# Optimization experiments

Hardware: AMD Instinct MI355X
Metric: run time of the kernel (lower is better)

The kernel has to match this reference:

```python
import jax, jax.numpy as jnp
import numpy as np

HIDDEN = 1024
HEADS = 16
DK = HIDDEN // HEADS  # 64
B, N = 2, 2048


def setup_inputs() -> dict:
    key = jax.random.key(0)
    ks = jax.random.split(key, 12)
    s = 0.02
    return {
        "q": jax.random.normal(ks[0], (B, N, HIDDEN), jnp.float32),
        "k": jax.random.normal(ks[1], (B, N, HIDDEN), jnp.float32),
        "v": jax.random.normal(ks[2], (B, N, HIDDEN), jnp.float32),
        "attn_bias": jax.random.normal(ks[3], (B, N, N), jnp.float32),
        "attention_mask": jnp.zeros((B, N, N), jnp.float32),
        # projection weights stored [in, out]
        "Wq": jax.random.normal(ks[4], (HIDDEN, HIDDEN), jnp.float32) * s,
        "bq": jnp.zeros((HIDDEN,), jnp.float32),
        "Wk": jax.random.normal(ks[5], (HIDDEN, HIDDEN), jnp.float32) * s,
        "bk": jnp.zeros((HIDDEN,), jnp.float32),
        "Wv": jax.random.normal(ks[6], (HIDDEN, HIDDEN), jnp.float32) * s,
        "bv": jnp.zeros((HIDDEN,), jnp.float32),
        "Wo": jax.random.normal(ks[7], (HIDDEN, HIDDEN), jnp.float32) * s,
        "bo": jnp.zeros((HIDDEN,), jnp.float32),
    }


def reference(q, k, v, attn_bias, attention_mask, Wq, bq, Wk, bk, Wv, bv, Wo, bo):
    b, n, _ = q.shape
    scale = DK ** (-0.5)
    # project and split heads: [B, H, N, Dk]
    qh = (q @ Wq + bq).reshape(b, n, HEADS, DK).transpose(0, 2, 1, 3)
    kh = (k @ Wk + bk).reshape(b, -1, HEADS, DK).transpose(0, 2, 1, 3)
    vh = (v @ Wv + bv).reshape(b, -1, HEADS, DK).transpose(0, 2, 1, 3)
    # scaled scores + additive bias/mask broadcast over heads: [B, H, N, N]
    scores = jnp.einsum('bhnd,bhmd->bhnm', qh * scale, kh)
    scores = scores + attn_bias[:, None, :, :] + attention_mask[:, None, :, :]
    probs = jax.nn.softmax(scores, axis=-1)  # dropout is identity at inference
    ctx = jnp.einsum('bhnm,bhmd->bhnd', probs, vh)
    ctx = ctx.transpose(0, 2, 1, 3).reshape(b, n, HEADS * DK)
    return ctx @ Wo + bo
```

## Files before the change

kernel.cpp:

```cpp
#include <hip/hip_runtime.h>
#include <hip/hip_bf16.h>

#define HIDDEN 1024
#define NHEADS 16
#define DKH   64
#define BATCH 2
#define SEQ   2048
#define MTOT  (BATCH*SEQ)

using bf16x8 = __attribute__((ext_vector_type(8))) short;
using f32x4  = __attribute__((ext_vector_type(4))) float;
using u16x4  = __attribute__((ext_vector_type(4))) unsigned short;

__device__ __forceinline__ unsigned short f2bf(float f) {
    union { __hip_bfloat16 h; unsigned short u; } v;
    v.h = __float2bfloat16(f);
    return v.u;
}

__device__ __forceinline__ float asfloat(unsigned int u) {
    union { unsigned int u; float f; } v; v.u = u; return v.f;
}

__device__ __forceinline__ float fexp2(float x) {
#if __has_builtin(__builtin_amdgcn_exp2f)
    return __builtin_amdgcn_exp2f(x);
#else
    return exp2f(x);
#endif
}

__device__ __forceinline__ void gload16(const unsigned short* g, unsigned short* l) {
    __builtin_amdgcn_global_load_lds((const __attribute__((address_space(1))) void*)g,
                                     (__attribute__((address_space(3))) void*)l, 16, 0, 0);
}

#define L2E 1.44269504088896340736f

__global__ __launch_bounds__(256) void prep(const float* __restrict__ Wq,
                                            const float* __restrict__ Wk,
                                            const float* __restrict__ Wv,
                                            const float* __restrict__ Wo,
                                            unsigned short* __restrict__ wt,
                                            const float* __restrict__ bias,
                                            const float* __restrict__ mask,
                                            unsigned short* __restrict__ biasf) {
    __shared__ __align__(16) char sh[16640];
    float (*tile)[65] = (float (*)[65])sh;
    unsigned short (*lb)[520] = (unsigned short (*)[520])sh;
    const int bid = blockIdx.x, t = threadIdx.x;
    if (bid >= 1024) {
        int r = bid - 1024;
        const int z = r >> 8; r &= 255;
        const int kb = (r >> 4) * 64, nb = (r & 15) * 64;
        const float* W = (z == 0) ? Wq : (z == 1) ? Wk : (z == 2) ? Wv : Wo;
        unsigned short* out = wt + (size_t)z * HIDDEN * HIDDEN;
        #pragma unroll
        for (int i = 0; i < 16; i++) {
            int idx = i * 256 + t; int rr = idx >> 6, c = idx & 63;
            tile[rr][c] = W[(size_t)(kb + rr) * HIDDEN + nb + c];
        }
        __syncthreads();
        #pragma unroll
        for (int i = 0; i < 16; i++) {
            int idx = i * 256 + t; int n = idx >> 6, kk = idx & 63;
            out[(size_t)(nb + n) * HIDDEN + kb + kk] = f2bf(tile[kk][n]);
        }
    } else {
        const int cb = bid;
        const int chunk = cb & 3, g = (cb >> 2) & 127, b = cb >> 9;
        const float* bp = bias + ((size_t)b * SEQ + g * 16) * SEQ + chunk * 512;
        const float* mp = mask + ((size_t)b * SEQ + g * 16) * SEQ + chunk * 512;
        #pragma unroll
        for (int i = 0; i < 8; i++) {
            int idx = i * 256 + t;
            int row = idx >> 7, c4 = (idx & 127) * 4;
            float4 bv4 = *(const float4*)(bp + (size_t)row * SEQ + c4);
            float4 mv4 = *(const float4*)(mp + (size_t)row * SEQ + c4);
            union { u16x4 v; unsigned short s[4]; } o;
            o.s[0] = f2bf((bv4.x + mv4.x) * L2E);
            o.s[1] = f2bf((bv4.y + mv4.y) * L2E);
            o.s[2] = f2bf((bv4.z + mv4.z) * L2E);
            o.s[3] = f2bf((bv4.w + mv4.w) * L2E);
            *(u16x4*)&lb[row][c4] = o.v;
        }
        __syncthreads();
        const int w = t >> 6, ln = t & 63;
        const int quad = ln >> 4, c16 = ln & 15;
        unsigned short* ob = biasf + (((size_t)b * 128 + g) * 64 + chunk * 16) * 512 + ln * 8;
        #pragma unroll
        for (int it = 0; it < 4; it++) {
            int ttl = it * 4 + w;
            *(bf16x8*)(ob + (size_t)ttl * 512) = *(const bf16x8*)&lb[c16][ttl * 32 + quad * 8];
        }
    }
}

template <bool AF32>
__device__ __forceinline__ void gemm_core_128_t(const void* __restrict__ Xv,
                                                const unsigned short* __restrict__ Wt,
                                                unsigned short* smem,
                                                int mbase, int nbase, f32x4 acc[4][4]) {
    const int tid = threadIdx.x, w = tid >> 6, ln = tid & 63;
    const int qr = (w >> 1) * 64, qc = (w & 1) * 64;
    const int g = ln >> 4, c16 = ln & 15;
    #pragma unroll
    for (int rt = 0; rt < 4; rt++)
        #pragma unroll
        for (int ct = 0; ct < 4; ct++) acc[rt][ct] = (f32x4){0.f, 0.f, 0.f, 0.f};

    const float* Xf = (const float*)Xv;
    const unsigned short* X16 = (const unsigned short*)Xv;
    float4 fa[4][2];
    if constexpr (AF32) {
        #pragma unroll
        for (int pass = 0; pass < 4; pass++) {
            int L = pass * 256 + tid;
            int r = L >> 3, cc = L & 7;
            const float* p = Xf + (size_t)(mbase + r) * HIDDEN + cc * 8;
            fa[pass][0] = *(const float4*)p;
            fa[pass][1] = *(const float4*)(p + 4);
        }
    }

    for (int kk = 0; kk < HIDDEN; kk += 64) {
        __syncthreads();
        if constexpr (AF32) {
            #pragma unroll
            for (int pass = 0; pass < 4; pass++) {
                int L = pass * 256 + tid;
                int r = L >> 3, c = (L & 7) ^ (r & 7);
                gload16(Wt + (size_t)(nbase + r) * HIDDEN + kk + c * 8,
                        smem + 8192 + (size_t)(pass * 256 + w * 64) * 8);
            }
            #pragma unroll
            for (int pass = 0; pass < 4; pass++) {
                int L = pass * 256 + tid;
                int r = L >> 3, cc = L & 7;
                int cs = cc ^ (r & 7);
                union { bf16x8 v; unsigned short s[8]; } o;
                o.s[0] = f2bf(fa[pass][0].x); o.s[1] = f2bf(fa[pass][0].y);
                o.s[2] = f2bf(fa[pass][0].z); o.s[3] = f2bf(fa[pass][0].w);
                o.s[4] = f2bf(fa[pass][1].x); o.s[5] = f2bf(fa[pass][1].y);
                o.s[6] = f2bf(fa[pass][1].z); o.s[7] = f2bf(fa[pass][1].w);
                *(bf16x8*)(smem + (size_t)(r * 8 + cs) * 8) = o.v;
            }
        } else {
            #pragma unroll
            for (int pass = 0; pass < 4; pass++) {
                int L = pass * 256 + tid;
                int r = L >> 3, c = (L & 7) ^ (r & 7);
                gload16(X16 + (size_t)(mbase + r) * HIDDEN + kk + c * 8,
                        smem + (size_t)(pass * 256 + w * 64) * 8);
                gload16(Wt + (size_t)(nbase + r) * HIDDEN + kk + c * 8,
                        smem + 8192 + (size_t)(pass * 256 + w * 64) * 8);
            }
        }
        __syncthreads();
        if constexpr (AF32) {
            if (kk + 64 < HIDDEN) {
                #pragma unroll
                for (int pass = 0; pass < 4; pass++) {
                    int L = pass * 256 + tid;
                    int r = L >> 3, cc = L & 7;
                    const float* p = Xf + (size_t)(mbase + r) * HIDDEN + (kk + 64) + cc * 8;
                    fa[pass][0] = *(const float4*)p;
                    fa[pass][1] = *(const float4*)(p + 4);
                }
            }
        }
        #pragma unroll
        for (int ks = 0; ks < 2; ks++) {
            bf16x8 af[4], bfr[4];
            #pragma unroll
            for (int rt = 0; rt < 4; rt++) {
                int r = qr + rt * 16 + c16;
                int ch = (g + ks * 4) ^ (r & 7);
                af[rt] = *(const bf16x8*)(smem + (size_t)(r * 8 + ch) * 8);
            }
            #pragma unroll
            for (int ct = 0; ct < 4; ct++) {
                int n = qc + ct * 16 + c16;
                int ch = (g + ks * 4) ^ (n & 7);
                bfr[ct] = *(const bf16x8*)(smem + 8192 + (size_t)(n * 8 + ch) * 8);
            }
            #pragma unroll
            for (int rt = 0; rt < 4; rt++)
                #pragma unroll
                for (int ct = 0; ct < 4; ct++)
                    acc[rt][ct] = __builtin_amdgcn_mfma_f32_16x16x32_bf16(af[rt], bfr[ct], acc[rt][ct], 0, 0, 0);
        }
    }
    __syncthreads();
}

__global__ __launch_bounds__(256, 2) void proj_gemm(const float* __restrict__ qf32,
                                                    const float* __restrict__ kf32,
                                                    const float* __restrict__ vf32,
                                                    const unsigned short* __restrict__ Wtall,
                                                    const float* __restrict__ bq,
                                                    const float* __restrict__ bk,
                                                    const float* __restrict__ bv,
                                                    unsigned short* __restrict__ qh,
                                                    unsigned short* __restrict__ khs,
                                                    unsigned short* __restrict__ vts) {
    __shared__ __align__(16) unsigned short smem[18432];
    const int z = blockIdx.z;
    const float* X  = (z == 0) ? qf32 : (z == 1) ? kf32 : vf32;
    const unsigned short* Wt = Wtall + (size_t)z * HIDDEN * HIDDEN;
    const float* bias = (z == 0) ? bq : (z == 1) ? bk : bv;
    const int mbase = blockIdx.x * 128, nbase = blockIdx.y * 128;
    const int tid = threadIdx.x, w = tid >> 6, ln = tid & 63;
    const int qr = (w >> 1) * 64, qc = (w & 1) * 64;
    const int g = ln >> 4, c16 = ln & 15;

    f32x4 acc[4][4];
    gemm_core_128_t<true>(X, Wt, smem, mbase, nbase, acc);

    const float scale = (z == 0) ? (0.125f * L2E) : 1.0f;
    float bias_v[4];
    #pragma unroll
    for (int ct = 0; ct < 4; ct++) bias_v[ct] = bias[nbase + qc + ct * 16 + c16];

    unsigned short* eld = smem + w * 4608;
    #pragma unroll
    for (int rt = 0; rt < 4; rt++)
        #pragma unroll
        for (int ct = 0; ct < 4; ct++)
            #pragma unroll
            for (int r4 = 0; r4 < 4; r4++) {
                int row_l = rt * 16 + g * 4 + r4;
                int col_l = ct * 16 + c16;
                float val = (acc[rt][ct][r4] + bias_v[ct]) * scale;
                if (z == 2) eld[col_l * 72 + row_l] = f2bf(val);
                else        eld[row_l * 72 + col_l] = f2bf(val);
            }
    __syncthreads();

    const int b = mbase >> 11;
    const int pos0 = (mbase & 2047) + qr;
    const int h = (nbase + qc) >> 6;
    const int bh = b * NHEADS + h;
    if (z == 0) {
        const int row8 = ln >> 3, col8 = (ln & 7) * 8;
        unsigned short* dst0 = qh + ((size_t)bh * SEQ + pos0) * DKH;
        #pragma unroll
        for (int j = 0; j < 8; j++) {
            int row = j * 8 + row8;
            *(bf16x8*)(dst0 + row * 64 + col8) = *(const bf16x8*)&eld[row * 72 + col8];
        }
    } else if (z == 1) {
        unsigned short* base = khs + ((size_t)bh * 64 + (pos0 >> 5)) * 2048;
        const int kvp = (c16 >> 2) * 8 + (c16 & 3);
        #pragma unroll
        for (int j = 0; j < 8; j++) {
            int tloc = j >> 2, ks = (j >> 1) & 1, kvs = j & 1;
            int kvl = tloc * 32 + kvp + kvs * 4;
            *(bf16x8*)(base + tloc * 2048 + ks * 1024 + kvs * 512 + ln * 8)
                = *(const bf16x8*)&eld[kvl * 72 + ks * 32 + g * 8];
        }
    } else {
        unsigned short* base = vts + ((size_t)bh * 64 + (pos0 >> 5)) * 2048;
        #pragma unroll
        for (int j = 0; j < 8; j++) {
            int tloc = j >> 2, dt = j & 3;
            *(bf16x8*)(base + tloc * 2048 + dt * 512 + ln * 8)
                = *(const bf16x8*)&eld[(dt * 16 + c16) * 72 + tloc * 32 + g * 8];
        }
    }
}

__global__ __launch_bounds__(256, 4) void attn(const unsigned short* __restrict__ qh,
                                               const unsigned short* __restrict__ khs,
                                               const unsigned short* __restrict__ vts,
                                               const unsigned short* __restrict__ biasf,
                                               unsigned short* __restrict__ ctx) {
    __shared__ __align__(16) unsigned short smem[16384];
    const int tid = threadIdx.x, w = tid >> 6, ln = tid & 63;
    const int quad = ln >> 4, c16 = ln & 15;
    const int bid = blockIdx.x;
    const int xcd = bid & 7, jj = bid >> 3;
    const int bh = xcd * 4 + (jj >> 5);
    const int qb = jj & 31;
    const int b = bh >> 4, h = bh & 15;

    bf16x8 qf[2];
    {
        const unsigned short* qp = qh + ((size_t)bh * SEQ + qb * 64 + w * 16 + c16) * DKH + quad * 8;
        qf[0] = *(const bf16x8*)qp;
        qf[1] = *(const bf16x8*)(qp + 32);
    }

    const unsigned short* kT = khs + (size_t)bh * 131072;
    const unsigned short* vT = vts + (size_t)bh * 131072;
    const unsigned short* bb = biasf + (((size_t)b * 128 + qb * 4 + w) * 64) * 512 + ln * 8;

    f32x4 accv[4];
    #pragma unroll
    for (int dt = 0; dt < 4; dt++) accv[dt] = (f32x4){0.f, 0.f, 0.f, 0.f};
    float lacc = 0.f;

    bf16x8 bcur[4];
    #pragma unroll
    for (int j = 0; j < 4; j++) bcur[j] = *(const bf16x8*)(bb + j * 512);

    for (int T = 0; T < 16; T++) {
        __syncthreads();
        {
            const unsigned short* ksrc = kT + T * 8192 + w * 512 + ln * 8;
            const unsigned short* vsrc = vT + T * 8192 + w * 512 + ln * 8;
            unsigned short* lk = smem + w * 512;
            unsigned short* lv = smem + 8192 + w * 512;
            #pragma unroll
            for (int p = 0; p < 4; p++) {
                gload16(ksrc + p * 2048, lk + p * 2048);
                gload16(vsrc + p * 2048, lv + p * 2048);
            }
        }
        bf16x8 bnext[4];
        {
            const int Tn = (T < 15) ? T + 1 : 15;
            #pragma unroll
            for (int j = 0; j < 4; j++)
                bnext[j] = *(const bf16x8*)(bb + (Tn * 4 + j) * 512);
        }
        __syncthreads();
        #pragma unroll
        for (int j = 0; j < 4; j++) {
            bf16x8 kf00 = *(const bf16x8*)(smem + j * 2048 + ln * 8);
            bf16x8 kf01 = *(const bf16x8*)(smem + j * 2048 + 512 + ln * 8);
            bf16x8 kf10 = *(const bf16x8*)(smem + j * 2048 + 1024 + ln * 8);
            bf16x8 kf11 = *(const bf16x8*)(smem + j * 2048 + 1536 + ln * 8);
            bf16x8 vf[4];
            #pragma unroll
            for (int dt = 0; dt < 4; dt++)
                vf[dt] = *(const bf16x8*)(smem + 8192 + j * 2048 + dt * 512 + ln * 8);
            const unsigned int* bd = (const unsigned int*)&bcur[j];
            f32x4 s0, s1;
            s0[0] = asfloat(bd[0] << 16); s0[1] = asfloat(bd[0] & 0xFFFF0000u);
            s0[2] = asfloat(bd[1] << 16); s0[3] = asfloat(bd[1] & 0xFFFF0000u);
            s1[0] = asfloat(bd[2] << 16); s1[1] = asfloat(bd[2] & 0xFFFF0000u);
            s1[2] = asfloat(bd[3] << 16); s1[3] = asfloat(bd[3] & 0xFFFF0000u);
            s0 = __builtin_amdgcn_mfma_f32_16x16x32_bf16(kf00, qf[0], s0, 0, 0, 0);
            s0 = __builtin_amdgcn_mfma_f32_16x16x32_bf16(kf10, qf[1], s0, 0, 0, 0);
            s1 = __builtin_amdgcn_mfma_f32_16x16x32_bf16(kf01, qf[0], s1, 0, 0, 0);
            s1 = __builtin_amdgcn_mfma_f32_16x16x32_bf16(kf11, qf[1], s1, 0, 0, 0);
            #pragma unroll
            for (int r = 0; r < 4; r++) { s0[r] = fexp2(s0[r]); s1[r] = fexp2(s1[r]); }
            lacc += ((s0[0] + s0[1]) + (s0[2] + s0[3]))
                  + ((s1[0] + s1[1]) + (s1[2] + s1[3]));
            union { bf16x8 v; __hip_bfloat162 hh[4]; } pu;
            pu.hh[0] = __float22bfloat162_rn(make_float2(s0[0], s0[1]));
            pu.hh[1] = __float22bfloat162_rn(make_float2(s0[2], s0[3]));
            pu.hh[2] = __float22bfloat162_rn(make_float2(s1[0], s1[1]));
            pu.hh[3] = __float22bfloat162_rn(make_float2(s1[2], s1[3]));
            #pragma unroll
            for (int dt = 0; dt < 4; dt++)
                accv[dt] = __builtin_amdgcn_mfma_f32_16x16x32_bf16(vf[dt], pu.v, accv[dt], 0, 0, 0);
            bcur[j] = bnext[j];
        }
    }

    float l = lacc;
    l += __shfl_xor(l, 16);
    l += __shfl_xor(l, 32);
    const float inv = 1.0f / l;
    __syncthreads();
    unsigned short* ot = smem + w * 1152;
    #pragma unroll
    for (int dt = 0; dt < 4; dt++)
        #pragma unroll
        for (int r = 0; r < 4; r += 2) {
            union { __hip_bfloat162 hh; unsigned int u; } pk;
            pk.hh = __float22bfloat162_rn(make_float2(accv[dt][r] * inv,
                                                     accv[dt][r + 1] * inv));
            *(unsigned int*)&ot[c16 * 72 + dt * 16 + quad * 4 + r] = pk.u;
        }
    const int row = ln >> 2, seg = ln & 3;
    const unsigned short* srcp = ot + row * 72 + seg * 16;
    unsigned short* dstp = ctx + ((size_t)b * SEQ + qb * 64 + w * 16 + row) * HIDDEN
                         + h * 64 + seg * 16;
    *(bf16x8*)(dstp)     = *(const bf16x8*)(srcp);
    *(bf16x8*)(dstp + 8) = *(const bf16x8*)(srcp + 8);
}

__global__ __launch_bounds__(256, 2) void outproj(const unsigned short* __restrict__ X,
                                                  const unsigned short* __restrict__ Wt,
                                                  const float* __restrict__ bo,
                                                  float* __restrict__ out) {
    __shared__ __align__(16) unsigned short smem[12288];
    const int mbase = blockIdx.x * 64, nbase = blockIdx.y * 128;
    const int tid = threadIdx.x, w = tid >> 6, ln = tid & 63;
    const int qr = (w >> 1) * 32, qc = (w & 1) * 64;
    const int g = ln >> 4, c16 = ln & 15;

    f32x4 acc[2][4];
    #pragma unroll
    for (int rt = 0; rt < 2; rt++)
        #pragma unroll
        for (int ct = 0; ct < 4; ct++) acc[rt][ct] = (f32x4){0.f, 0.f, 0.f, 0.f};

    for (int kk = 0; kk < HIDDEN; kk += 64) {
        __syncthreads();
        #pragma unroll
        for (int pass = 0; pass < 2; pass++) {
            int L = pass * 256 + tid;
            int r = L >> 3, c = (L & 7) ^ (r & 7);
            gload16(X + (size_t)(mbase + r) * HIDDEN + kk + c * 8,
                    smem + (size_t)(pass * 256 + w * 64) * 8);
        }
        #pragma unroll
        for (int pass = 0; pass < 4; pass++) {
            int L = pass * 256 + tid;
            int r = L >> 3, c = (L & 7) ^ (r & 7);
            gload16(Wt + (size_t)(nbase + r) * HIDDEN + kk + c * 8,
                    smem + 4096 + (size_t)(pass * 256 + w * 64) * 8);
        }
        __syncthreads();
        #pragma unroll
        for (int ks = 0; ks < 2; ks++) {
            bf16x8 af[2], bfr[4];
            #pragma unroll
            for (int rt = 0; rt < 2; rt++) {
                int r = qr + rt * 16 + c16;
                int ch = (g + ks * 4) ^ (r & 7);
                af[rt] = *(const bf16x8*)(smem + (size_t)(r * 8 + ch) * 8);
            }
            #pragma unroll
            for (int ct = 0; ct < 4; ct++) {
                int n = qc + ct * 16 + c16;
                int ch = (g + ks * 4) ^ (n & 7);
                bfr[ct] = *(const bf16x8*)(smem + 4096 + (size_t)(n * 8 + ch) * 8);
            }
            #pragma unroll
            for (int rt = 0; rt < 2; rt++)
                #pragma unroll
                for (int ct = 0; ct < 4; ct++)
                    acc[rt][ct] = __builtin_amdgcn_mfma_f32_16x16x32_bf16(af[rt], bfr[ct], acc[rt][ct], 0, 0, 0);
        }
    }

    float bo_v[4];
    #pragma unroll
    for (int ct = 0; ct < 4; ct++) bo_v[ct] = bo[nbase + qc + ct * 16 + c16];
    #pragma unroll
    for (int rt = 0; rt < 2; rt++)
        #pragma unroll
        for (int ct = 0; ct < 4; ct++)
            #pragma unroll
            for (int r4 = 0; r4 < 4; r4++)
                out[(size_t)(mbase + qr + rt * 16 + g * 4 + r4) * HIDDEN + nbase + qc + ct * 16 + c16]
                    = acc[rt][ct][r4] + bo_v[ct];
}

extern "C" void kernel_launch(void* const* d_in, const int* in_sizes, int n_in,
                              void* d_out, int out_size, void* d_ws, size_t ws_size,
                              hipStream_t stream) {
    const float* q    = (const float*)d_in[0];
    const float* k    = (const float*)d_in[1];
    const float* v    = (const float*)d_in[2];
    const float* bias = (const float*)d_in[3];
    const float* mask = (const float*)d_in[4];
    const float* Wq   = (const float*)d_in[5];
    const float* bq   = (const float*)d_in[6];
    const float* Wk   = (const float*)d_in[7];
    const float* bk   = (const float*)d_in[8];
    const float* Wv   = (const float*)d_in[9];
    const float* bv   = (const float*)d_in[10];
    const float* Wo   = (const float*)d_in[11];
    const float* bo   = (const float*)d_in[12];

    char* ws = (char*)d_ws;
    unsigned short* wt     = (unsigned short*)(ws + 25165824);
    unsigned short* qh     = (unsigned short*)(ws + 33554432);
    unsigned short* khs    = (unsigned short*)(ws + 41943040);
    unsigned short* vts    = (unsigned short*)(ws + 50331648);
    unsigned short* ctx    = (unsigned short*)(ws + 58720256);
    unsigned short* biasf  = (unsigned short*)(ws + 67108864);

    prep<<<2048, 256, 0, stream>>>(Wq, Wk, Wv, Wo, wt, bias, mask, biasf);
    proj_gemm<<<dim3(32, 8, 3), 256, 0, stream>>>(q, k, v, wt, bq, bk, bv, qh, khs, vts);
    attn<<<1024, 256, 0, stream>>>(qh, khs, vts, biasf, ctx);
    outproj<<<dim3(64, 8), 256, 0, stream>>>(ctx, wt + (size_t)3 * HIDDEN * HIDDEN, bo,
                                             (float*)d_out);
}
```

Before: 268.2 us.

## Store bias in fp32 and compute softmax denominator via MFMA with ones

The combined bias+mask tile is now stored as fp32 instead of bf16, so the attention kernel loads it straight into the MFMA accumulators and no longer unpacks bf16 by shift and mask. The scalar row-sum of exponentials plus its cross-lane shuffles is replaced by one extra MFMA against a vector of bf16 ones, which also makes the denominator use the same bf16-rounded probabilities as the numerator. The bias prefetch for the next tile is removed and the loads are issued inside the same iteration. In exchange, bias traffic doubles in both prep and attn, and the workspace layout moves to make room for the larger buffer.

```diff
diff --git a/kernel.cpp b/kernel.cpp
--- a/kernel.cpp
+++ b/kernel.cpp
@@ -16,10 +16,6 @@
     union { __hip_bfloat16 h; unsigned short u; } v;
     v.h = __float2bfloat16(f);
     return v.u;
-}
-
-__device__ __forceinline__ float asfloat(unsigned int u) {
-    union { unsigned int u; float f; } v; v.u = u; return v.f;
 }
 
 __device__ __forceinline__ float fexp2(float x) {
@@ -44,10 +40,10 @@
                                             unsigned short* __restrict__ wt,
                                             const float* __restrict__ bias,
                                             const float* __restrict__ mask,
-                                            unsigned short* __restrict__ biasf) {
-    __shared__ __align__(16) char sh[16640];
+                                            float* __restrict__ biasf) {
+    __shared__ __align__(16) char sh[33536];
     float (*tile)[65] = (float (*)[65])sh;
-    unsigned short (*lb)[520] = (unsigned short (*)[520])sh;
+    float (*lbf)[524] = (float (*)[524])sh;
     const int bid = blockIdx.x, t = threadIdx.x;
     if (bid >= 1024) {
         int r = bid - 1024;
@@ -77,21 +73,21 @@
             int row = idx >> 7, c4 = (idx & 127) * 4;
             float4 bv4 = *(const float4*)(bp + (size_t)row * SEQ + c4);
             float4 mv4 = *(const float4*)(mp + (size_t)row * SEQ + c4);
-            union { u16x4 v; unsigned short s[4]; } o;
-            o.s[0] = f2bf((bv4.x + mv4.x) * L2E);
-            o.s[1] = f2bf((bv4.y + mv4.y) * L2E);
-            o.s[2] = f2bf((bv4.z + mv4.z) * L2E);
-            o.s[3] = f2bf((bv4.w + mv4.w) * L2E);
-            *(u16x4*)&lb[row][c4] = o.v;
+            float4 o;
+            o.x = (bv4.x + mv4.x) * L2E; o.y = (bv4.y + mv4.y) * L2E;
+            o.z = (bv4.z + mv4.z) * L2E; o.w = (bv4.w + mv4.w) * L2E;
+            *(float4*)&lbf[row][c4] = o;
         }
         __syncthreads();
         const int w = t >> 6, ln = t & 63;
         const int quad = ln >> 4, c16 = ln & 15;
-        unsigned short* ob = biasf + (((size_t)b * 128 + g) * 64 + chunk * 16) * 512 + ln * 8;
+        float* ob = biasf + (((size_t)b * 128 + g) * 64 + chunk * 16) * 512 + ln * 8;
         #pragma unroll
         for (int it = 0; it < 4; it++) {
             int ttl = it * 4 + w;
-            *(bf16x8*)(ob + (size_t)ttl * 512) = *(const bf16x8*)&lb[c16][ttl * 32 + quad * 8];
+            const float* src = &lbf[c16][ttl * 32 + quad * 8];
+            *(f32x4*)(ob + (size_t)ttl * 512)     = *(const f32x4*)src;
+            *(f32x4*)(ob + (size_t)ttl * 512 + 4) = *(const f32x4*)(src + 4);
         }
     }
 }
@@ -273,7 +269,7 @@
 __global__ __launch_bounds__(256, 4) void attn(const unsigned short* __restrict__ qh,
                                                const unsigned short* __restrict__ khs,
                                                const unsigned short* __restrict__ vts,
-                                               const unsigned short* __restrict__ biasf,
+                                               const float* __restrict__ biasf,
                                                unsigned short* __restrict__ ctx) {
     __shared__ __align__(16) unsigned short smem[16384];
     const int tid = threadIdx.x, w = tid >> 6, ln = tid & 63;
@@ -293,16 +289,15 @@
 
     const unsigned short* kT = khs + (size_t)bh * 131072;
     const unsigned short* vT = vts + (size_t)bh * 131072;
-    const unsigned short* bb = biasf + (((size_t)b * 128 + qb * 4 + w) * 64) * 512 + ln * 8;
+    const float* bb = biasf + ((size_t)(b * 128 + qb * 4 + w) * 64) * 512 + ln * 8;
+
+    const short one_bf = (short)0x3F80;
+    bf16x8 vones = {one_bf, one_bf, one_bf, one_bf, one_bf, one_bf, one_bf, one_bf};
 
     f32x4 accv[4];
     #pragma unroll
     for (int dt = 0; dt < 4; dt++) accv[dt] = (f32x4){0.f, 0.f, 0.f, 0.f};
-    float lacc = 0.f;
-
-    bf16x8 bcur[4];
-    #pragma unroll
-    for (int j = 0; j < 4; j++) bcur[j] = *(const bf16x8*)(bb + j * 512);
+    f32x4 dsum = (f32x4){0.f, 0.f, 0.f, 0.f};
 
     for (int T = 0; T < 16; T++) {
         __syncthreads();
@@ -317,12 +312,12 @@
                 gload16(vsrc + p * 2048, lv + p * 2048);
             }
         }
-        bf16x8 bnext[4];
-        {
-            const int Tn = (T < 15) ? T + 1 : 15;
-            #pragma unroll
-            for (int j = 0; j < 4; j++)
-                bnext[j] = *(const bf16x8*)(bb + (Tn * 4 + j) * 512);
+        f32x4 bc0[4], bc1[4];
+        #pragma unroll
+        for (int j = 0; j < 4; j++) {
+            const float* bp_ = bb + (size_t)(T * 4 + j) * 512;
+            bc0[j] = *(const f32x4*)bp_;
+            bc1[j] = *(const f32x4*)(bp_ + 4);
         }
         __syncthreads();
         #pragma unroll
@@ -335,36 +330,26 @@
             #pragma unroll
             for (int dt = 0; dt < 4; dt++)
                 vf[dt] = *(const bf16x8*)(smem + 8192 + j * 2048 + dt * 512 + ln * 8);
-            const unsigned int* bd = (const unsigned int*)&bcur[j];
-            f32x4 s0, s1;
-            s0[0] = asfloat(bd[0] << 16); s0[1] = asfloat(bd[0] & 0xFFFF0000u);
-            s0[2] = asfloat(bd[1] << 16); s0[3] = asfloat(bd[1] & 0xFFFF0000u);
-            s1[0] = asfloat(bd[2] << 16); s1[1] = asfloat(bd[2] & 0xFFFF0000u);
-            s1[2] = asfloat(bd[3] << 16); s1[3] = asfloat(bd[3] & 0xFFFF0000u);
+            f32x4 s0 = bc0[j], s1 = bc1[j];
             s0 = __builtin_amdgcn_mfma_f32_16x16x32_bf16(kf00, qf[0], s0, 0, 0, 0);
             s0 = __builtin_amdgcn_mfma_f32_16x16x32_bf16(kf10, qf[1], s0, 0, 0, 0);
             s1 = __builtin_amdgcn_mfma_f32_16x16x32_bf16(kf01, qf[0], s1, 0, 0, 0);
             s1 = __builtin_amdgcn_mfma_f32_16x16x32_bf16(kf11, qf[1], s1, 0, 0, 0);
             #pragma unroll
             for (int r = 0; r < 4; r++) { s0[r] = fexp2(s0[r]); s1[r] = fexp2(s1[r]); }
-            lacc += ((s0[0] + s0[1]) + (s0[2] + s0[3]))
-                  + ((s1[0] + s1[1]) + (s1[2] + s1[3]));
             union { bf16x8 v; __hip_bfloat162 hh[4]; } pu;
             pu.hh[0] = __float22bfloat162_rn(make_float2(s0[0], s0[1]));
             pu.hh[1] = __float22bfloat162_rn(make_float2(s0[2], s0[3]));
             pu.hh[2] = __float22bfloat162_rn(make_float2(s1[0], s1[1]));
             pu.hh[3] = __float22bfloat162_rn(make_float2(s1[2], s1[3]));
+            dsum = __builtin_amdgcn_mfma_f32_16x16x32_bf16(vones, pu.v, dsum, 0, 0, 0);
             #pragma unroll
             for (int dt = 0; dt < 4; dt++)
                 accv[dt] = __builtin_amdgcn_mfma_f32_16x16x32_bf16(vf[dt], pu.v, accv[dt], 0, 0, 0);
-            bcur[j] = bnext[j];
-        }
-    }
-
-    float l = lacc;
-    l += __shfl_xor(l, 16);
-    l += __shfl_xor(l, 32);
-    const float inv = 1.0f / l;
+        }
+    }
+
+    const float inv = 1.0f / dsum[0];
     __syncthreads();
     unsigned short* ot = smem + w * 1152;
     #pragma unroll
@@ -471,12 +456,12 @@
     const float* bo   = (const float*)d_in[12];
 
     char* ws = (char*)d_ws;
-    unsigned short* wt     = (unsigned short*)(ws + 25165824);
-    unsigned short* qh     = (unsigned short*)(ws + 33554432);
-    unsigned short* khs    = (unsigned short*)(ws + 41943040);
-    unsigned short* vts    = (unsigned short*)(ws + 50331648);
-    unsigned short* ctx    = (unsigned short*)(ws + 58720256);
-    unsigned short* biasf  = (unsigned short*)(ws + 67108864);
+    float*          biasf  = (float*)ws;
+    unsigned short* wt     = (unsigned short*)(ws + 33554432);
+    unsigned short* qh     = (unsigned short*)(ws + 41943040);
+    unsigned short* khs    = (unsigned short*)(ws + 50331648);
+    unsigned short* vts    = (unsigned short*)(ws + 58720256);
+    unsigned short* ctx    = (unsigned short*)(ws + 67108864);
 
     prep<<<2048, 256, 0, stream>>>(Wq, Wk, Wv, Wo, wt, bias, mask, biasf);
     proj_gemm<<<dim3(32, 8, 3), 256, 0, stream>>>(q, k, v, wt, bq, bk, bv, qh, khs, vts);
```

Result: slower. 290.5 us (+8.3%).
